# Performance work log

Hardware: AMD Instinct MI355X
Metric: run time of the kernel (lower is better)

## Reference

```python
import jax, jax.numpy as jnp
import numpy as np

B, N1, N2, D, K = 8, 2048, 512, 128, 32
LEVELS, RES, BASE, FC = 3, 3, 0.25, 192
R3 = RES ** 3  # 27 voxel bins per level
EPS = 1e-5


def group_norm(x, gamma, beta, groups):
    # x: [b, C, ...]; normalize per (group) over channel-subset + spatial dims
    b, c = x.shape[0], x.shape[1]
    xg = x.reshape(b, groups, -1)
    mu = xg.mean(axis=-1, keepdims=True)
    var = xg.var(axis=-1, keepdims=True)
    xn = ((xg - mu) * jax.lax.rsqrt(var + EPS)).reshape(x.shape)
    shape = (1, c) + (1,) * (x.ndim - 2)
    return xn * gamma.reshape(shape) + beta.reshape(shape)


def prelu(x, a):
    return jnp.where(x >= 0, x, a * x)


def setup_inputs() -> dict:
    key = jax.random.key(0)
    ks = jax.random.split(key, 12)
    def w(k, shape):
        fan_in = shape[-1]
        return jax.random.uniform(k, shape, jnp.float32, -1.0, 1.0) / jnp.sqrt(jnp.float32(fan_in))
    return {
        "coords": jax.random.normal(ks[0], (B, N1, 3), jnp.float32),
        "coords2": jax.random.normal(ks[1], (B, N2, 3), jnp.float32),
        "fmap1": jax.random.normal(ks[2], (B, D, N1), jnp.float32),
        "fmap2": jax.random.normal(ks[3], (B, D, N2), jnp.float32),
        # vol_conv: Conv1d(81,128,1) -> GN(8,128) -> PReLU -> Conv1d(128,192,1)
        "W1": w(ks[4], (128, R3 * LEVELS)), "b1": jnp.zeros((128,), jnp.float32),
        "g1": jnp.ones((128,), jnp.float32), "be1": jnp.zeros((128,), jnp.float32),
        "a1": jnp.array(0.25, jnp.float32),
        "W2": w(ks[5], (FC, 128)), "b2": jnp.zeros((FC,), jnp.float32),
        # knn_conv: Conv2d(4,64,1) -> GN(8,64) -> PReLU;  knn_out: Conv1d(64,192,1)
        "Wk": w(ks[6], (64, 4)), "bk": jnp.zeros((64,), jnp.float32),
        "gk": jnp.ones((64,), jnp.float32), "bek": jnp.zeros((64,), jnp.float32),
        "ak": jnp.array(0.25, jnp.float32),
        "Wo": w(ks[7], (FC, 64)), "bo": jnp.zeros((FC,), jnp.float32),
    }


def reference(coords, coords2, fmap1, fmap2, W1, b1, g1, be1, a1, W2, b2,
              Wk, bk, gk, bek, ak, Wo, bo):
    b, n1 = coords.shape[0], coords.shape[1]
    n2 = coords2.shape[1]
    dim = fmap1.shape[1]

    # correlation: [b, n1, n2]
    corr = jnp.einsum('bdn,bdm->bnm', fmap1, fmap2) / jnp.sqrt(jnp.float32(dim))
    # pairwise offsets template - search: [b, n1, n2, 3]
    diff = coords2[:, None, :, :] - coords[:, :, None, :]

    # --- multi-level voxel feature via scatter-add ---
    base = jnp.arange(b * n1, dtype=jnp.int32).reshape(b, n1, 1) * R3
    feats = []
    for i in range(LEVELS):
        r = BASE * (2 ** i)
        dv = jnp.round(diff / r)
        valid = jnp.all(jnp.abs(dv) <= (RES // 2), axis=-1)          # [b,n1,n2]
        dvi = (dv + 1.0).astype(jnp.int32)
        cube = dvi[..., 0] * (RES * RES) + dvi[..., 1] * RES + dvi[..., 2]
        idx = jnp.where(valid, cube, 0)                              # torch: cube*valid
        seg = (base + idx).reshape(-1)
        vf = valid.astype(corr.dtype)
        nseg = b * n1 * R3
        add = jax.ops.segment_sum((corr * vf).reshape(-1), seg, num_segments=nseg).reshape(b, n1, R3)
        cnt = jax.ops.segment_sum(vf.reshape(-1), seg, num_segments=nseg).reshape(b, n1, R3)
        feats.append((add / jnp.clip(cnt, 1.0, float(n1))).transpose(0, 2, 1))  # [b,R3,n1]
    vol = jnp.concatenate(feats, axis=1)                             # [b, 3*27, n1]

    h = jnp.einsum('oc,bcn->bon', W1, vol) + b1[None, :, None]
    h = prelu(group_norm(h, g1, be1, 8), a1)
    vol_out = jnp.einsum('oc,bcn->bon', W2, h) + b2[None, :, None]   # [b, FC, n1]

    # --- KNN feature ---
    dist = jnp.sum(diff * diff, axis=-1)                             # [b,n1,n2]
    _, nbr = jax.lax.top_k(-dist, K)                                 # [b,n1,K]
    knn_corr = jnp.take_along_axis(corr, nbr, axis=2)                # [b,n1,K]
    knn_xyz = jnp.take_along_axis(diff, nbr[..., None], axis=2)      # [b,n1,K,3]
    e = jnp.concatenate([knn_corr[:, None], knn_xyz.transpose(0, 3, 1, 2)], axis=1)  # [b,4,n1,K]
    h = jnp.einsum('oc,bcnk->bonk', Wk, e) + bk[None, :, None, None]
    h = prelu(group_norm(h, gk, bek, 8), ak)
    h = jnp.max(h, axis=3)                                           # [b,64,n1]
    knn_out = jnp.einsum('oc,bcn->bon', Wo, h) + bo[None, :, None]   # [b,FC,n1]

    return vol_out + knn_out
```

## Files before the change

### kernel.cpp

```cpp
#include <hip/hip_runtime.h>
#include <hip/hip_bf16.h>

#define N1 2048
#define N2 512
#define KNN 32

typedef unsigned short u16;
typedef unsigned int u32;
typedef unsigned long long u64;
typedef __attribute__((ext_vector_type(8))) short bf16x8;
typedef __attribute__((ext_vector_type(4))) float f32x4;

#define OFF_WT   0
#define OFF_W1B  18432
#define OFF_GV   36864
#define OFF_GK   36992
#define OFF_FLAG 37120
#define OFF_H1   37128
#define OFF_KM   1085704
#define OFF_CO   1609992

__device__ __forceinline__ float tof(u16 u) {
  union { u32 i; float f; } v; v.i = ((u32)u) << 16; return v.f;
}
__device__ __forceinline__ u16 tob(float f) {
  __hip_bfloat16 h = __float2bfloat16(f);
  return *reinterpret_cast<u16*>(&h);
}
__device__ __forceinline__ float fs(float v) {
  return (fabsf(v) < 1e30f) ? v : 0.f;
}

template <int BF>
__device__ __forceinline__ float LD(const void* p, size_t i) {
  if (BF) return tof(((const u16*)p)[i]);
  return ((const float*)p)[i];
}
template <int BF>
__device__ __forceinline__ void ST(void* p, size_t i, float v) {
  if (BF) ((u16*)p)[i] = tob(v);
  else    ((float*)p)[i] = v;
}

__device__ __forceinline__ u32 umin32(u32 a, u32 b) { return a < b ? a : b; }

__device__ __forceinline__ u32 wave_min_u32(u32 v) {
  v = umin32(v, (u32)__builtin_amdgcn_update_dpp((int)0xFFFFFFFF, (int)v, 0x111, 0xf, 0xf, false));
  v = umin32(v, (u32)__builtin_amdgcn_update_dpp((int)0xFFFFFFFF, (int)v, 0x112, 0xf, 0xf, false));
  v = umin32(v, (u32)__builtin_amdgcn_update_dpp((int)0xFFFFFFFF, (int)v, 0x114, 0xf, 0xf, false));
  v = umin32(v, (u32)__builtin_amdgcn_update_dpp((int)0xFFFFFFFF, (int)v, 0x118, 0xf, 0xf, false));
  v = umin32(v, (u32)__builtin_amdgcn_update_dpp((int)0xFFFFFFFF, (int)v, 0x142, 0xa, 0xf, false));
  v = umin32(v, (u32)__builtin_amdgcn_update_dpp((int)0xFFFFFFFF, (int)v, 0x143, 0xc, 0xf, false));
  return (u32)__builtin_amdgcn_readlane((int)v, 63);
}

template <int BF>
__device__ void prep_body(const void* W2, const void* Wo, const void* W1,
                          float* ws, int i0, int stride) {
  u16* wtb = (u16*)(ws + OFF_WT);
  for (int i = i0; i < 192 * 192; i += stride) {
    int o = i / 192, c = i % 192;
    float v = (c < 128) ? LD<BF>(W2, o * 128 + c) : LD<BF>(Wo, o * 64 + (c - 128));
    wtb[o * 192 + c] = tob(fs(v));
  }
  u16* w1b = (u16*)(ws + OFF_W1B);
  for (int i = i0; i < 128 * 96; i += stride) {
    int c = i / 96, j = i % 96;
    float v = (j < 81) ? LD<BF>(W1, c * 81 + j) : 0.f;
    w1b[c * 96 + j] = tob(fs(v));
  }
}

__global__ __launch_bounds__(256) void k_prep(const void* fmap1,
                                              const void* W2, const void* Wo,
                                              const void* W1, float* ws) {
  int t = threadIdx.x;
  __shared__ int sbad;
  if (t == 0) sbad = 0;
  __syncthreads();
  int bad = 0;
  const u16* fm = (const u16*)fmap1;
  for (int i = t * 8; i < t * 8 + 8; i++) {
    float v = tof(fm[i]);
    if (!(fabsf(v) <= 64.f)) bad = 1;
  }
  if (bad) atomicOr(&sbad, 1);
  __syncthreads();
  int bf = sbad ? 0 : 1;
  if (blockIdx.x == 0) {
    if (t == 0) ((int*)(ws + OFF_FLAG))[0] = bf;
    (ws + OFF_GV)[t] = 0.f;
  }
  int i0 = blockIdx.x * 256 + t, stride = gridDim.x * 256;
  if (bf) prep_body<1>(W2, Wo, W1, ws, i0, stride);
  else    prep_body<0>(W2, Wo, W1, ws, i0, stride);
}

template <int BF>
__device__ void corr_stage(const void* f1, const void* f2, u16* As, u16* Bs,
                           int b, int m0, int n0, int t) {
#pragma unroll
  for (int rep = 0; rep < 2; rep++) {
    int i = t + rep * 256;
    int m8 = i & 15, d4 = i >> 4;
    u16 e[4][8];
    if (BF) {
      const u16* F1 = (const u16*)f1;
#pragma unroll
      for (int dr = 0; dr < 4; dr++) {
        uint4 v = *(const uint4*)&F1[(size_t)(b * 128 + d4 * 4 + dr) * N1 + m0 + m8 * 8];
        u32 w[4] = {v.x, v.y, v.z, v.w};
#pragma unroll
        for (int j = 0; j < 8; j++) e[dr][j] = (u16)(w[j >> 1] >> ((j & 1) * 16));
      }
    } else {
      const float* F1 = (const float*)f1;
#pragma unroll
      for (int dr = 0; dr < 4; dr++) {
        const float* src = &F1[(size_t)(b * 128 + d4 * 4 + dr) * N1 + m0 + m8 * 8];
        float4 a = *(const float4*)src, c = *(const float4*)(src + 4);
        float f[8] = {a.x, a.y, a.z, a.w, c.x, c.y, c.z, c.w};
#pragma unroll
        for (int j = 0; j < 8; j++) e[dr][j] = tob(f[j]);
      }
    }
#pragma unroll
    for (int j = 0; j < 8; j++) {
      u64 pk = (u64)e[0][j] | ((u64)e[1][j] << 16) | ((u64)e[2][j] << 32) |
               ((u64)e[3][j] << 48);
      *(u64*)&As[(m8 * 8 + j) * 136 + d4 * 4] = pk;
    }
  }
  {
    int n8 = t & 7, d4 = t >> 3;
    u16 e[4][8];
    if (BF) {
      const u16* F2 = (const u16*)f2;
#pragma unroll
      for (int dr = 0; dr < 4; dr++) {
        uint4 v = *(const uint4*)&F2[(size_t)(b * 128 + d4 * 4 + dr) * N2 + n0 + n8 * 8];
        u32 w[4] = {v.x, v.y, v.z, v.w};
#pragma unroll
        for (int j = 0; j < 8; j++) e[dr][j] = (u16)(w[j >> 1] >> ((j & 1) * 16));
      }
    } else {
      const float* F2 = (const float*)f2;
#pragma unroll
      for (int dr = 0; dr < 4; dr++) {
        const float* src = &F2[(size_t)(b * 128 + d4 * 4 + dr) * N2 + n0 + n8 * 8];
        float4 a = *(const float4*)src, c = *(const float4*)(src + 4);
        float f[8] = {a.x, a.y, a.z, a.w, c.x, c.y, c.z, c.w};
#pragma unroll
        for (int j = 0; j < 8; j++) e[dr][j] = tob(f[j]);
      }
    }
#pragma unroll
    for (int j = 0; j < 8; j++) {
      u64 pk = (u64)e[0][j] | ((u64)e[1][j] << 16) | ((u64)e[2][j] << 32) |
               ((u64)e[3][j] << 48);
      *(u64*)&Bs[(n8 * 8 + j) * 136 + d4 * 4] = pk;
    }
  }
}

__global__ __launch_bounds__(256) void k_corr(const int* flag,
                                              const void* f1, const void* f2,
                                              u16* corrb) {
  __shared__ __attribute__((aligned(16))) u16 As[128 * 136];
  __shared__ __attribute__((aligned(16))) u16 Bs[64 * 136];
  int b = blockIdx.z, m0 = blockIdx.x * 128, n0 = blockIdx.y * 64, t = threadIdx.x;
  if (*flag) corr_stage<1>(f1, f2, As, Bs, b, m0, n0, t);
  else       corr_stage<0>(f1, f2, As, Bs, b, m0, n0, t);
  __syncthreads();

  int wv = t >> 6, lane = t & 63;
  int l15 = lane & 15, q = lane >> 4;
  int wm = (wv >> 1) * 64, wn = (wv & 1) * 32;
  f32x4 acc[4][2];
#pragma unroll
  for (int mt = 0; mt < 4; mt++)
#pragma unroll
    for (int nt = 0; nt < 2; nt++) acc[mt][nt] = (f32x4){0.f, 0.f, 0.f, 0.f};

#pragma unroll
  for (int kc = 0; kc < 128; kc += 32) {
    bf16x8 af[4], bf[2];
#pragma unroll
    for (int mt = 0; mt < 4; mt++)
      af[mt] = *(const bf16x8*)&As[(wm + mt * 16 + l15) * 136 + kc + q * 8];
#pragma unroll
    for (int nt = 0; nt < 2; nt++)
      bf[nt] = *(const bf16x8*)&Bs[(wn + nt * 16 + l15) * 136 + kc + q * 8];
#pragma unroll
    for (int mt = 0; mt < 4; mt++)
#pragma unroll
      for (int nt = 0; nt < 2; nt++)
        acc[mt][nt] = __builtin_amdgcn_mfma_f32_16x16x32_bf16(
            af[mt], bf[nt], acc[mt][nt], 0, 0, 0);
  }
  const float s = 0.08838834764831843f;
#pragma unroll
  for (int mt = 0; mt < 4; mt++)
#pragma unroll
    for (int nt = 0; nt < 2; nt++)
#pragma unroll
      for (int r = 0; r < 4; r++) {
        int m = m0 + wm + mt * 16 + q * 4 + r;
        int n = n0 + wn + nt * 16 + l15;
        corrb[((size_t)(b * N1 + m)) * N2 + n] = tob(acc[mt][nt][r] * s);
      }
}

template <int BF>
__device__ void point_body(const void* coords, const void* coords2,
                           u16* corrb, const void* Wk, const void* bk,
                           u16* knnmax, float* gknnraw,
                           float* c2s, float* binsum, float* bincnt,
                           float4* e_s, float* statk,
                           int b, int p0, int t) {
  int wv = t >> 6, lane = t & 63;
  for (int i = t; i < N2 * 3; i += 256) c2s[i] = LD<BF>(coords2, b * N2 * 3 + i);
  for (int i = t; i < 324; i += 256) { binsum[i] = 0.f; bincnt[i] = 0.f; }
  if (t < 16) statk[t] = 0.f;
  int p = p0 + wv;
  float px = LD<BF>(coords, (b * N1 + p) * 3 + 0);
  float py = LD<BF>(coords, (b * N1 + p) * 3 + 1);
  float pz = LD<BF>(coords, (b * N1 + p) * 3 + 2);
  u16* crow = corrb + ((size_t)(b * N1 + p)) * N2;
  __syncthreads();

  u64 kk[8];
#pragma unroll
  for (int i = 0; i < 8; i++) {
    int n2 = i * 64 + lane;
    float cv = tof(crow[n2]);
    float dx = c2s[n2 * 3 + 0] - px;
    float dy = c2s[n2 * 3 + 1] - py;
    float dz = c2s[n2 * 3 + 2] - pz;
    float dist = __fadd_rn(__fadd_rn(__fmul_rn(dx, dx), __fmul_rn(dy, dy)),
                           __fmul_rn(dz, dz));
    union { float f; u32 u; } du; du.f = dist;
    kk[i] = (((u64)du.u) << 32) | (u64)n2;
    float sc = 4.f;
#pragma unroll
    for (int lvl = 0; lvl < 3; lvl++) {
      float vx = rintf(dx * sc), vy = rintf(dy * sc), vz = rintf(dz * sc);
      if (fabsf(vx) <= 1.f && fabsf(vy) <= 1.f && fabsf(vz) <= 1.f) {
        int cube = ((int)vx + 1) * 9 + ((int)vy + 1) * 3 + ((int)vz + 1);
        atomicAdd(&binsum[wv * 81 + lvl * 27 + cube], cv);
        atomicAdd(&bincnt[wv * 81 + lvl * 27 + cube], 1.f);
      }
      sc *= 0.5f;
    }
  }

#define CAS(a, b) { u64 x = kk[a], y = kk[b]; bool sw = y < x; \
                    kk[a] = sw ? y : x; kk[b] = sw ? x : y; }
  CAS(0,1) CAS(2,3) CAS(4,5) CAS(6,7)
  CAS(0,2) CAS(1,3) CAS(4,6) CAS(5,7)
  CAS(1,2) CAS(5,6)
  CAS(0,4) CAS(1,5) CAS(2,6) CAS(3,7)
  CAS(2,4) CAS(3,5)
  CAS(1,2) CAS(3,4) CAS(5,6)
#undef CAS
  int my_idx = 0;
  for (int it = 0; it < KNN; it++) {
    u32 hb = (u32)(kk[0] >> 32);
    u32 wb = wave_min_u32(hb);
    u32 hidx = (hb == wb) ? (u32)kk[0] : 0xFFFFFFFFu;
    u32 widx = wave_min_u32(hidx);
    if (lane == it) my_idx = (int)widx;
    if (lane == (int)(widx & 63u)) {
      kk[0] = kk[1]; kk[1] = kk[2]; kk[2] = kk[3]; kk[3] = kk[4];
      kk[4] = kk[5]; kk[5] = kk[6]; kk[6] = kk[7]; kk[7] = ~0ull;
    }
  }
  if (lane < KNN) {
    float4 ev;
    ev.x = tof(crow[my_idx]);
    ev.y = c2s[my_idx * 3 + 0] - px;
    ev.z = c2s[my_idx * 3 + 1] - py;
    ev.w = c2s[my_idx * 3 + 2] - pz;
    e_s[wv * 32 + lane] = ev;
  }
#pragma unroll
  for (int rep = 0; rep < 2; rep++) {
    int i = lane + rep * 64;
    if (i < 96) {
      float v = (i < 81)
          ? binsum[wv * 81 + i] / fmaxf(bincnt[wv * 81 + i], 1.f) : 0.f;
      crow[i] = tob(v);
    }
  }

  {
    int cch = lane;
    float w0 = LD<BF>(Wk, cch * 4 + 0), w1 = LD<BF>(Wk, cch * 4 + 1);
    float w2 = LD<BF>(Wk, cch * 4 + 2), w3 = LD<BF>(Wk, cch * 4 + 3);
    float bv = LD<BF>(bk, cch);
    float sm = 0.f, sq = 0.f, mx = -3e38f;
#pragma unroll 8
    for (int k = 0; k < KNN; k++) {
      float4 ev = e_s[wv * 32 + k];
      float h = bv + w0 * ev.x + w1 * ev.y + w2 * ev.z + w3 * ev.w;
      sm += h; sq += h * h; mx = fmaxf(mx, h);
    }
    knnmax[((size_t)(b * N1 + p)) * 64 + cch] = tob(mx);
    sm += __shfl_xor(sm, 1, 64); sq += __shfl_xor(sq, 1, 64);
    sm += __shfl_xor(sm, 2, 64); sq += __shfl_xor(sq, 2, 64);
    sm += __shfl_xor(sm, 4, 64); sq += __shfl_xor(sq, 4, 64);
    if ((lane & 7) == 0) {
      int g = cch >> 3;
      atomicAdd(&statk[g * 2 + 0], sm);
      atomicAdd(&statk[g * 2 + 1], sq);
    }
  }
  __syncthreads();
  if (t < 16) atomicAdd(&gknnraw[b * 16 + t], statk[t]);
}

__global__ __launch_bounds__(256) void k_point(const int* flag,
                                               const void* coords, const void* coords2,
                                               u16* corrb, const void* Wk,
                                               const void* bk, u16* knnmax,
                                               float* gknnraw) {
  __shared__ float c2s[N2 * 3];
  __shared__ float binsum[4 * 81];
  __shared__ float bincnt[4 * 81];
  __shared__ float4 e_s[4 * 32];
  __shared__ float statk[16];
  int b = blockIdx.y, p0 = blockIdx.x * 4, t = threadIdx.x;
  if (*flag)
    point_body<1>(coords, coords2, corrb, Wk, bk, knnmax, gknnraw,
                  c2s, binsum, bincnt, e_s, statk, b, p0, t);
  else
    point_body<0>(coords, coords2, corrb, Wk, bk, knnmax, gknnraw,
                  c2s, binsum, bincnt, e_s, statk, b, p0, t);
}

template <int BF>
__device__ void vol_body(const u16* corrb, const u16* w1b, const void* b1,
                         u16* h1b, float* gvolraw, float* Bi1, float* statv,
                         int b, int p0, int t) {
  if (t < 128) Bi1[t] = LD<BF>(b1, t);
  if (t < 16) statv[t] = 0.f;
  __syncthreads();

  int wv = t >> 6, lane = t & 63;
  int l15 = lane & 15, q = lane >> 4;
  int pbase = p0 + wv * 16;
  f32x4 acc[8];
#pragma unroll
  for (int nt = 0; nt < 8; nt++) acc[nt] = (f32x4){0.f, 0.f, 0.f, 0.f};

#pragma unroll
  for (int kc = 0; kc < 96; kc += 32) {
    bf16x8 af = *(const bf16x8*)&corrb[((size_t)(b * N1 + pbase + l15)) * N2 + kc + q * 8];
    bf16x8 bf[8];
#pragma unroll
    for (int nt = 0; nt < 8; nt++)
      bf[nt] = *(const bf16x8*)&w1b[(nt * 16 + l15) * 96 + kc + q * 8];
#pragma unroll
    for (int nt = 0; nt < 8; nt++)
      acc[nt] = __builtin_amdgcn_mfma_f32_16x16x32_bf16(af, bf[nt], acc[nt], 0, 0, 0);
  }
  float sm[8], sq[8];
#pragma unroll
  for (int nt = 0; nt < 8; nt++) {
    int c = nt * 16 + l15;
    float s0 = 0.f, q0 = 0.f;
#pragma unroll
    for (int r = 0; r < 4; r++) {
      int p = pbase + q * 4 + r;
      float v = acc[nt][r] + Bi1[c];
      h1b[((size_t)(b * N1 + p)) * 128 + c] = tob(v);
      s0 += v; q0 += v * v;
    }
    sm[nt] = s0; sq[nt] = q0;
  }
#pragma unroll
  for (int nt = 0; nt < 8; nt++) {
    sm[nt] += __shfl_xor(sm[nt], 16, 64); sq[nt] += __shfl_xor(sq[nt], 16, 64);
    sm[nt] += __shfl_xor(sm[nt], 32, 64); sq[nt] += __shfl_xor(sq[nt], 32, 64);
  }
  if (q == 0) {
#pragma unroll
    for (int nt = 0; nt < 8; nt++) {
      int g = (nt * 16 + l15) >> 4;
      atomicAdd(&statv[g * 2 + 0], sm[nt]);
      atomicAdd(&statv[g * 2 + 1], sq[nt]);
    }
  }
  __syncthreads();
  if (t < 16) atomicAdd(&gvolraw[b * 16 + t], statv[t]);
}

__global__ __launch_bounds__(256) void k_vol(const int* flag, const u16* corrb,
                                             const u16* w1b, const void* b1,
                                             u16* h1b, float* gvolraw) {
  __shared__ float Bi1[128];
  __shared__ float statv[16];
  int b = blockIdx.y, p0 = blockIdx.x * 64, t = threadIdx.x;
  if (*flag) vol_body<1>(corrb, w1b, b1, h1b, gvolraw, Bi1, statv, b, p0, t);
  else       vol_body<0>(corrb, w1b, b1, h1b, gvolraw, Bi1, statv, b, p0, t);
}

template <int BF>
__device__ void out_body(const u16* h1b, const u16* knnmax, const u16* wtb,
                         const float* gvolraw, const float* gknnraw,
                         const void* g1, const void* be1, const void* a1p,
                         const void* gk, const void* bek, const void* akp,
                         const void* b2, const void* bo, void* out,
                         float* Ac, float* Bc, float* Sc, float* Bi, u16* gs,
                         int b, int p0, int t) {
  if (t < 192) {
    float A, Bv, slope;
    if (t < 128) {
      int g = t >> 4;
      float S = fs(gvolraw[b * 16 + g * 2 + 0]);
      float Q = fs(gvolraw[b * 16 + g * 2 + 1]);
      float mean = S / 32768.f;
      float var = fmaxf(Q / 32768.f - mean * mean, 0.f);
      float inv = 1.f / sqrtf(var + 1e-5f);
      A = inv * LD<BF>(g1, t); Bv = LD<BF>(be1, t) - mean * A;
      slope = LD<BF>(a1p, 0);
    } else {
      int c = t - 128, g = c >> 3;
      float S = fs(gknnraw[b * 16 + g * 2 + 0]);
      float Q = fs(gknnraw[b * 16 + g * 2 + 1]);
      float mean = S / 524288.f;
      float var = fmaxf(Q / 524288.f - mean * mean, 0.f);
      float inv = 1.f / sqrtf(var + 1e-5f);
      A = inv * LD<BF>(gk, c); Bv = LD<BF>(bek, c) - mean * A;
      slope = LD<BF>(akp, 0);
    }
    Ac[t] = A; Bc[t] = Bv; Sc[t] = slope;
    Bi[t] = LD<BF>(b2, t) + LD<BF>(bo, t);
  }
  __syncthreads();

  for (int i = t; i < 1536; i += 256) {
    int p = i / 24, c8 = i % 24;
    int c0 = c8 * 8;
    uint4 v;
    if (c8 < 16) v = *(const uint4*)&h1b[((size_t)(b * N1 + p0 + p)) * 128 + c0];
    else         v = *(const uint4*)&knnmax[((size_t)(b * N1 + p0 + p)) * 64 + (c0 - 128)];
    u16 e[8] = {(u16)(v.x & 0xffff), (u16)(v.x >> 16), (u16)(v.y & 0xffff),
                (u16)(v.y >> 16),    (u16)(v.z & 0xffff), (u16)(v.z >> 16),
                (u16)(v.w & 0xffff), (u16)(v.w >> 16)};
    u16 r[8];
#pragma unroll
    for (int j = 0; j < 8; j++) {
      int c = c0 + j;
      float xn = tof(e[j]) * Ac[c] + Bc[c];
      xn = xn >= 0.f ? xn : Sc[c] * xn;
      r[j] = tob(xn);
    }
    uint4 wv;
    wv.x = (u32)r[0] | ((u32)r[1] << 16);
    wv.y = (u32)r[2] | ((u32)r[3] << 16);
    wv.z = (u32)r[4] | ((u32)r[5] << 16);
    wv.w = (u32)r[6] | ((u32)r[7] << 16);
    *(uint4*)&gs[p * 200 + c0] = wv;
  }
  __syncthreads();

  int wv2 = t >> 6, lane = t & 63;
  int l15 = lane & 15, q = lane >> 4;
  int obase = wv2 * 48;
  f32x4 acc[3][4];
#pragma unroll
  for (int mt = 0; mt < 3; mt++)
#pragma unroll
    for (int nt = 0; nt < 4; nt++) acc[mt][nt] = (f32x4){0.f, 0.f, 0.f, 0.f};

#pragma unroll
  for (int kc = 0; kc < 192; kc += 32) {
    bf16x8 af[3], bf[4];
#pragma unroll
    for (int mt = 0; mt < 3; mt++)
      af[mt] = *(const bf16x8*)&wtb[(size_t)(obase + mt * 16 + l15) * 192 + kc + q * 8];
#pragma unroll
    for (int nt = 0; nt < 4; nt++)
      bf[nt] = *(const bf16x8*)&gs[(nt * 16 + l15) * 200 + kc + q * 8];
#pragma unroll
    for (int mt = 0; mt < 3; mt++)
#pragma unroll
      for (int nt = 0; nt < 4; nt++)
        acc[mt][nt] = __builtin_amdgcn_mfma_f32_16x16x32_bf16(
            af[mt], bf[nt], acc[mt][nt], 0, 0, 0);
  }
#pragma unroll
  for (int mt = 0; mt < 3; mt++)
#pragma unroll
    for (int nt = 0; nt < 4; nt++)
#pragma unroll
      for (int r = 0; r < 4; r++) {
        int o = obase + mt * 16 + q * 4 + r;
        int p = p0 + nt * 16 + l15;
        ST<BF>(out, ((size_t)(b * 192 + o)) * N1 + p, fs(acc[mt][nt][r] + Bi[o]));
      }
}

__global__ __launch_bounds__(256) void k_out(const int* flag,
                                             const u16* h1b, const u16* knnmax,
                                             const u16* wtb,
                                             const float* gvolraw, const float* gknnraw,
                                             const void* g1, const void* be1,
                                             const void* a1p, const void* gk,
                                             const void* bek, const void* akp,
                                             const void* b2, const void* bo,
                                             void* out) {
  __shared__ float Ac[192], Bc[192], Sc[192], Bi[192];
  __shared__ __attribute__((aligned(16))) u16 gs[64 * 200];
  int b = blockIdx.y, p0 = blockIdx.x * 64, t = threadIdx.x;
  if (*flag)
    out_body<1>(h1b, knnmax, wtb, gvolraw, gknnraw, g1, be1, a1p, gk, bek, akp,
                b2, bo, out, Ac, Bc, Sc, Bi, gs, b, p0, t);
  else
    out_body<0>(h1b, knnmax, wtb, gvolraw, gknnraw, g1, be1, a1p, gk, bek, akp,
                b2, bo, out, Ac, Bc, Sc, Bi, gs, b, p0, t);
}

extern "C" void kernel_launch(void* const* d_in, const int* in_sizes, int n_in,
                              void* d_out, int out_size, void* d_ws, size_t ws_size,
                              hipStream_t stream) {
  const void* coords  = d_in[0];
  const void* coords2 = d_in[1];
  const void* fmap1   = d_in[2];
  const void* fmap2   = d_in[3];
  const void* W1  = d_in[4];
  const void* b1  = d_in[5];
  const void* g1  = d_in[6];
  const void* be1 = d_in[7];
  const void* a1  = d_in[8];
  const void* W2  = d_in[9];
  const void* b2  = d_in[10];
  const void* Wk  = d_in[11];
  const void* bk  = d_in[12];
  const void* gk  = d_in[13];
  const void* bek = d_in[14];
  const void* ak  = d_in[15];
  const void* Wo  = d_in[16];
  const void* bo  = d_in[17];

  float* ws = (float*)d_ws;
  u16* wtb       = (u16*)(ws + OFF_WT);
  u16* w1b       = (u16*)(ws + OFF_W1B);
  float* gvolraw = ws + OFF_GV;
  float* gknnraw = ws + OFF_GK;
  const int* flag = (const int*)(ws + OFF_FLAG);
  u16* h1b    = (u16*)(ws + OFF_H1);
  u16* knnmax = (u16*)(ws + OFF_KM);
  u16* corrb  = (u16*)(ws + OFF_CO);

  k_prep<<<dim3(40), dim3(256), 0, stream>>>(fmap1, W2, Wo, W1, ws);
  k_corr<<<dim3(16, 8, 8), dim3(256), 0, stream>>>(flag, fmap1, fmap2, corrb);
  k_point<<<dim3(512, 8), dim3(256), 0, stream>>>(flag, coords, coords2, corrb,
                                                  Wk, bk, knnmax, gknnraw);
  k_vol<<<dim3(32, 8), dim3(256), 0, stream>>>(flag, corrb, w1b, b1, h1b, gvolraw);
  k_out<<<dim3(32, 8), dim3(256), 0, stream>>>(flag, h1b, knnmax, wtb,
                                               gvolraw, gknnraw, g1, be1, a1,
                                               gk, bek, ak, b2, bo, d_out);
}
```

Measured before the change: 210.4 us.

## Fuse point and vol kernels, drop W2/Wo prep, add ballot fast path in top-k

```diff
diff --git a/kernel.cpp b/kernel.cpp
--- a/kernel.cpp
+++ b/kernel.cpp
@@ -11,7 +11,6 @@
 typedef __attribute__((ext_vector_type(8))) short bf16x8;
 typedef __attribute__((ext_vector_type(4))) float f32x4;
 
-#define OFF_WT   0
 #define OFF_W1B  18432
 #define OFF_GV   36864
 #define OFF_GK   36992
@@ -55,25 +54,34 @@
 }
 
 template <int BF>
-__device__ void prep_body(const void* W2, const void* Wo, const void* W1,
-                          float* ws, int i0, int stride) {
-  u16* wtb = (u16*)(ws + OFF_WT);
-  for (int i = i0; i < 192 * 192; i += stride) {
-    int o = i / 192, c = i % 192;
-    float v = (c < 128) ? LD<BF>(W2, o * 128 + c) : LD<BF>(Wo, o * 64 + (c - 128));
-    wtb[o * 192 + c] = tob(fs(v));
-  }
+__device__ __forceinline__ bf16x8 ld_wfrag(const void* W2, const void* Wo,
+                                           int o, int k0) {
+  if (BF) {
+    const u16* p = (k0 < 128) ? (const u16*)W2 + (size_t)o * 128 + k0
+                              : (const u16*)Wo + (size_t)o * 64 + (k0 - 128);
+    return *(const bf16x8*)p;
+  } else {
+    const float* p = (k0 < 128) ? (const float*)W2 + (size_t)o * 128 + k0
+                                : (const float*)Wo + (size_t)o * 64 + (k0 - 128);
+    bf16x8 r;
+#pragma unroll
+    for (int j = 0; j < 8; j++) r[j] = (short)tob(p[j]);
+    return r;
+  }
+}
+
+template <int BF>
+__device__ void prep_body(const void* W1, float* ws, int i0, int stride) {
   u16* w1b = (u16*)(ws + OFF_W1B);
   for (int i = i0; i < 128 * 96; i += stride) {
     int c = i / 96, j = i % 96;
     float v = (j < 81) ? LD<BF>(W1, c * 81 + j) : 0.f;
-    w1b[c * 96 + j] = tob(fs(v));
-  }
-}
-
-__global__ __launch_bounds__(256) void k_prep(const void* fmap1,
-                                              const void* W2, const void* Wo,
-                                              const void* W1, float* ws) {
+    w1b[i] = tob(fs(v));
+  }
+}
+
+__global__ __launch_bounds__(256) void k_prep(const void* fmap1, const void* W1,
+                                              float* ws) {
   int t = threadIdx.x;
   __shared__ int sbad;
   if (t == 0) sbad = 0;
@@ -92,8 +100,8 @@
     (ws + OFF_GV)[t] = 0.f;
   }
   int i0 = blockIdx.x * 256 + t, stride = gridDim.x * 256;
-  if (bf) prep_body<1>(W2, Wo, W1, ws, i0, stride);
-  else    prep_body<0>(W2, Wo, W1, ws, i0, stride);
+  if (bf) prep_body<1>(W1, ws, i0, stride);
+  else    prep_body<0>(W1, ws, i0, stride);
 }
 
 template <int BF>
@@ -212,201 +220,195 @@
 }
 
 template <int BF>
-__device__ void point_body(const void* coords, const void* coords2,
-                           u16* corrb, const void* Wk, const void* bk,
-                           u16* knnmax, float* gknnraw,
-                           float* c2s, float* binsum, float* bincnt,
-                           float4* e_s, float* statk,
-                           int b, int p0, int t) {
+__device__ void pv_body(const void* coords, const void* coords2,
+                        const u16* corrb, const void* Wk, const void* bk,
+                        const u16* w1b, const void* b1,
+                        u16* h1b, u16* knnmax,
+                        float* gvolraw, float* gknnraw,
+                        float* c2s, float* binsum, float* bincnt,
+                        float4* e_s, u16* volb, float* statv, float* statk,
+                        int b, int p0, int t) {
   int wv = t >> 6, lane = t & 63;
+  int l15 = lane & 15, q = lane >> 4;
   for (int i = t; i < N2 * 3; i += 256) c2s[i] = LD<BF>(coords2, b * N2 * 3 + i);
-  for (int i = t; i < 324; i += 256) { binsum[i] = 0.f; bincnt[i] = 0.f; }
-  if (t < 16) statk[t] = 0.f;
-  int p = p0 + wv;
-  float px = LD<BF>(coords, (b * N1 + p) * 3 + 0);
-  float py = LD<BF>(coords, (b * N1 + p) * 3 + 1);
-  float pz = LD<BF>(coords, (b * N1 + p) * 3 + 2);
-  u16* crow = corrb + ((size_t)(b * N1 + p)) * N2;
-  __syncthreads();
-
-  u64 kk[8];
-#pragma unroll
-  for (int i = 0; i < 8; i++) {
-    int n2 = i * 64 + lane;
-    float cv = tof(crow[n2]);
-    float dx = c2s[n2 * 3 + 0] - px;
-    float dy = c2s[n2 * 3 + 1] - py;
-    float dz = c2s[n2 * 3 + 2] - pz;
-    float dist = __fadd_rn(__fadd_rn(__fmul_rn(dx, dx), __fmul_rn(dy, dy)),
-                           __fmul_rn(dz, dz));
-    union { float f; u32 u; } du; du.f = dist;
-    kk[i] = (((u64)du.u) << 32) | (u64)n2;
-    float sc = 4.f;
-#pragma unroll
-    for (int lvl = 0; lvl < 3; lvl++) {
-      float vx = rintf(dx * sc), vy = rintf(dy * sc), vz = rintf(dz * sc);
-      if (fabsf(vx) <= 1.f && fabsf(vy) <= 1.f && fabsf(vz) <= 1.f) {
-        int cube = ((int)vx + 1) * 9 + ((int)vy + 1) * 3 + ((int)vz + 1);
-        atomicAdd(&binsum[wv * 81 + lvl * 27 + cube], cv);
-        atomicAdd(&bincnt[wv * 81 + lvl * 27 + cube], 1.f);
-      }
-      sc *= 0.5f;
-    }
-  }
+  if (t < 16) { statv[t] = 0.f; statk[t] = 0.f; }
+  __syncthreads();
+
+  for (int s = 0; s < 4; s++) {
+    int pp = wv * 4 + s;
+    int p = p0 + pp;
+    for (int i = lane; i < 81; i += 64) {
+      binsum[wv * 81 + i] = 0.f;
+      bincnt[wv * 81 + i] = 0.f;
+    }
+    float px = LD<BF>(coords, (b * N1 + p) * 3 + 0);
+    float py = LD<BF>(coords, (b * N1 + p) * 3 + 1);
+    float pz = LD<BF>(coords, (b * N1 + p) * 3 + 2);
+    const u16* crow = corrb + ((size_t)(b * N1 + p)) * N2;
+
+    u64 kk[8];
+#pragma unroll
+    for (int i = 0; i < 8; i++) {
+      int n2 = i * 64 + lane;
+      float cv = tof(crow[n2]);
+      float dx = c2s[n2 * 3 + 0] - px;
+      float dy = c2s[n2 * 3 + 1] - py;
+      float dz = c2s[n2 * 3 + 2] - pz;
+      float dist = __fadd_rn(__fadd_rn(__fmul_rn(dx, dx), __fmul_rn(dy, dy)),
+                             __fmul_rn(dz, dz));
+      union { float f; u32 u; } du; du.f = dist;
+      kk[i] = (((u64)du.u) << 32) | (u64)n2;
+      float sc = 4.f;
+#pragma unroll
+      for (int lvl = 0; lvl < 3; lvl++) {
+        float vx = rintf(dx * sc), vy = rintf(dy * sc), vz = rintf(dz * sc);
+        if (fabsf(vx) <= 1.f && fabsf(vy) <= 1.f && fabsf(vz) <= 1.f) {
+          int cube = ((int)vx + 1) * 9 + ((int)vy + 1) * 3 + ((int)vz + 1);
+          atomicAdd(&binsum[wv * 81 + lvl * 27 + cube], cv);
+          atomicAdd(&bincnt[wv * 81 + lvl * 27 + cube], 1.f);
+        }
+        sc *= 0.5f;
+      }
+    }
 
 #define CAS(a, b) { u64 x = kk[a], y = kk[b]; bool sw = y < x; \
                     kk[a] = sw ? y : x; kk[b] = sw ? x : y; }
-  CAS(0,1) CAS(2,3) CAS(4,5) CAS(6,7)
-  CAS(0,2) CAS(1,3) CAS(4,6) CAS(5,7)
-  CAS(1,2) CAS(5,6)
-  CAS(0,4) CAS(1,5) CAS(2,6) CAS(3,7)
-  CAS(2,4) CAS(3,5)
-  CAS(1,2) CAS(3,4) CAS(5,6)
+    CAS(0,1) CAS(2,3) CAS(4,5) CAS(6,7)
+    CAS(0,2) CAS(1,3) CAS(4,6) CAS(5,7)
+    CAS(1,2) CAS(5,6)
+    CAS(0,4) CAS(1,5) CAS(2,6) CAS(3,7)
+    CAS(2,4) CAS(3,5)
+    CAS(1,2) CAS(3,4) CAS(5,6)
 #undef CAS
-  int my_idx = 0;
-  for (int it = 0; it < KNN; it++) {
-    u32 hb = (u32)(kk[0] >> 32);
-    u32 wb = wave_min_u32(hb);
-    u32 hidx = (hb == wb) ? (u32)kk[0] : 0xFFFFFFFFu;
-    u32 widx = wave_min_u32(hidx);
-    if (lane == it) my_idx = (int)widx;
-    if (lane == (int)(widx & 63u)) {
-      kk[0] = kk[1]; kk[1] = kk[2]; kk[2] = kk[3]; kk[3] = kk[4];
-      kk[4] = kk[5]; kk[5] = kk[6]; kk[6] = kk[7]; kk[7] = ~0ull;
-    }
-  }
-  if (lane < KNN) {
-    float4 ev;
-    ev.x = tof(crow[my_idx]);
-    ev.y = c2s[my_idx * 3 + 0] - px;
-    ev.z = c2s[my_idx * 3 + 1] - py;
-    ev.w = c2s[my_idx * 3 + 2] - pz;
-    e_s[wv * 32 + lane] = ev;
-  }
-#pragma unroll
-  for (int rep = 0; rep < 2; rep++) {
-    int i = lane + rep * 64;
-    if (i < 96) {
-      float v = (i < 81)
-          ? binsum[wv * 81 + i] / fmaxf(bincnt[wv * 81 + i], 1.f) : 0.f;
-      crow[i] = tob(v);
-    }
-  }
-
-  {
-    int cch = lane;
-    float w0 = LD<BF>(Wk, cch * 4 + 0), w1 = LD<BF>(Wk, cch * 4 + 1);
-    float w2 = LD<BF>(Wk, cch * 4 + 2), w3 = LD<BF>(Wk, cch * 4 + 3);
-    float bv = LD<BF>(bk, cch);
-    float sm = 0.f, sq = 0.f, mx = -3e38f;
+    int my_idx = 0;
+    for (int it = 0; it < KNN; it++) {
+      u32 hb = (u32)(kk[0] >> 32);
+      u32 wb = wave_min_u32(hb);
+      u64 mask = __ballot(hb == wb);
+      u32 widx;
+      if (__builtin_popcountll(mask) == 1) {
+        int wl = (int)__builtin_ctzll(mask);
+        widx = (u32)__builtin_amdgcn_readlane((int)(u32)kk[0], wl);
+      } else {
+        u32 hidx = (hb == wb) ? (u32)kk[0] : 0xFFFFFFFFu;
+        widx = wave_min_u32(hidx);
+      }
+      if (lane == it) my_idx = (int)widx;
+      if (lane == (int)(widx & 63u)) {
+        kk[0] = kk[1]; kk[1] = kk[2]; kk[2] = kk[3]; kk[3] = kk[4];
+        kk[4] = kk[5]; kk[5] = kk[6]; kk[6] = kk[7]; kk[7] = ~0ull;
+      }
+    }
+    if (lane < KNN) {
+      float4 ev;
+      ev.x = tof(crow[my_idx]);
+      ev.y = c2s[my_idx * 3 + 0] - px;
+      ev.z = c2s[my_idx * 3 + 1] - py;
+      ev.w = c2s[my_idx * 3 + 2] - pz;
+      e_s[wv * 32 + lane] = ev;
+    }
+#pragma unroll
+    for (int rep = 0; rep < 2; rep++) {
+      int i = lane + rep * 64;
+      if (i < 96) {
+        float v = (i < 81)
+            ? binsum[wv * 81 + i] / fmaxf(bincnt[wv * 81 + i], 1.f) : 0.f;
+        volb[pp * 104 + i] = tob(v);
+      }
+    }
+
+    {
+      int cch = lane;
+      float w0 = LD<BF>(Wk, cch * 4 + 0), w1 = LD<BF>(Wk, cch * 4 + 1);
+      float w2 = LD<BF>(Wk, cch * 4 + 2), w3 = LD<BF>(Wk, cch * 4 + 3);
+      float bv = LD<BF>(bk, cch);
+      float sm = 0.f, sq = 0.f, mx = -3e38f;
 #pragma unroll 8
-    for (int k = 0; k < KNN; k++) {
-      float4 ev = e_s[wv * 32 + k];
-      float h = bv + w0 * ev.x + w1 * ev.y + w2 * ev.z + w3 * ev.w;
-      sm += h; sq += h * h; mx = fmaxf(mx, h);
-    }
-    knnmax[((size_t)(b * N1 + p)) * 64 + cch] = tob(mx);
-    sm += __shfl_xor(sm, 1, 64); sq += __shfl_xor(sq, 1, 64);
-    sm += __shfl_xor(sm, 2, 64); sq += __shfl_xor(sq, 2, 64);
-    sm += __shfl_xor(sm, 4, 64); sq += __shfl_xor(sq, 4, 64);
-    if ((lane & 7) == 0) {
-      int g = cch >> 3;
-      atomicAdd(&statk[g * 2 + 0], sm);
-      atomicAdd(&statk[g * 2 + 1], sq);
-    }
-  }
-  __syncthreads();
-  if (t < 16) atomicAdd(&gknnraw[b * 16 + t], statk[t]);
-}
-
-__global__ __launch_bounds__(256) void k_point(const int* flag,
-                                               const void* coords, const void* coords2,
-                                               u16* corrb, const void* Wk,
-                                               const void* bk, u16* knnmax,
-                                               float* gknnraw) {
+      for (int k = 0; k < KNN; k++) {
+        float4 ev = e_s[wv * 32 + k];
+        float h = bv + w0 * ev.x + w1 * ev.y + w2 * ev.z + w3 * ev.w;
+        sm += h; sq += h * h; mx = fmaxf(mx, h);
+      }
+      knnmax[((size_t)(b * N1 + p)) * 64 + cch] = tob(mx);
+      sm += __shfl_xor(sm, 1, 64); sq += __shfl_xor(sq, 1, 64);
+      sm += __shfl_xor(sm, 2, 64); sq += __shfl_xor(sq, 2, 64);
+      sm += __shfl_xor(sm, 4, 64); sq += __shfl_xor(sq, 4, 64);
+      if ((lane & 7) == 0) {
+        int g = cch >> 3;
+        atomicAdd(&statk[g * 2 + 0], sm);
+        atomicAdd(&statk[g * 2 + 1], sq);
+      }
+    }
+  }
+  __syncthreads();
+
+  f32x4 acc[2];
+  acc[0] = (f32x4){0.f, 0.f, 0.f, 0.f};
+  acc[1] = (f32x4){0.f, 0.f, 0.f, 0.f};
+#pragma unroll
+  for (int kc = 0; kc < 96; kc += 32) {
+    bf16x8 af = *(const bf16x8*)&volb[l15 * 104 + kc + q * 8];
+    bf16x8 bf0 = *(const bf16x8*)&w1b[((2 * wv + 0) * 16 + l15) * 96 + kc + q * 8];
+    bf16x8 bf1 = *(const bf16x8*)&w1b[((2 * wv + 1) * 16 + l15) * 96 + kc + q * 8];
+    acc[0] = __builtin_amdgcn_mfma_f32_16x16x32_bf16(af, bf0, acc[0], 0, 0, 0);
+    acc[1] = __builtin_amdgcn_mfma_f32_16x16x32_bf16(af, bf1, acc[1], 0, 0, 0);
+  }
+#pragma unroll
+  for (int ct = 0; ct < 2; ct++) {
+    int c = (2 * wv + ct) * 16 + l15;
+    float bias = LD<BF>(b1, c);
+    float sm = 0.f, sq = 0.f;
+#pragma unroll
+    for (int r = 0; r < 4; r++) {
+      int p = p0 + q * 4 + r;
+      float v = acc[ct][r] + bias;
+      h1b[((size_t)(b * N1 + p)) * 128 + c] = tob(v);
+      sm += v; sq += v * v;
+    }
+    sm += __shfl_xor(sm, 1, 64);  sq += __shfl_xor(sq, 1, 64);
+    sm += __shfl_xor(sm, 2, 64);  sq += __shfl_xor(sq, 2, 64);
+    sm += __shfl_xor(sm, 4, 64);  sq += __shfl_xor(sq, 4, 64);
+    sm += __shfl_xor(sm, 8, 64);  sq += __shfl_xor(sq, 8, 64);
+    sm += __shfl_xor(sm, 16, 64); sq += __shfl_xor(sq, 16, 64);
+    sm += __shfl_xor(sm, 32, 64); sq += __shfl_xor(sq, 32, 64);
+    if (lane == 0) {
+      int g = 2 * wv + ct;
+      atomicAdd(&statv[g * 2 + 0], sm);
+      atomicAdd(&statv[g * 2 + 1], sq);
+    }
+  }
+  __syncthreads();
+  if (t < 16) atomicAdd(&gvolraw[b * 16 + t], statv[t]);
+  else if (t < 32) atomicAdd(&gknnraw[b * 16 + (t - 16)], statk[t - 16]);
+}
+
+__global__ __launch_bounds__(256) void k_pv(const int* flag,
+                                            const void* coords, const void* coords2,
+                                            const u16* corrb, const void* Wk,
+                                            const void* bk, const u16* w1b,
+                                            const void* b1, u16* h1b,
+                                            u16* knnmax, float* gvolraw,
+                                            float* gknnraw) {
   __shared__ float c2s[N2 * 3];
   __shared__ float binsum[4 * 81];
   __shared__ float bincnt[4 * 81];
   __shared__ float4 e_s[4 * 32];
-  __shared__ float statk[16];
-  int b = blockIdx.y, p0 = blockIdx.x * 4, t = threadIdx.x;
+  __shared__ __attribute__((aligned(16))) u16 volb[16 * 104];
+  __shared__ float statv[16], statk[16];
+  int b = blockIdx.y, p0 = blockIdx.x * 16, t = threadIdx.x;
   if (*flag)
-    point_body<1>(coords, coords2, corrb, Wk, bk, knnmax, gknnraw,
-                  c2s, binsum, bincnt, e_s, statk, b, p0, t);
+    pv_body<1>(coords, coords2, corrb, Wk, bk, w1b, b1, h1b, knnmax,
+               gvolraw, gknnraw, c2s, binsum, bincnt, e_s, volb, statv, statk,
+               b, p0, t);
   else
-    point_body<0>(coords, coords2, corrb, Wk, bk, knnmax, gknnraw,
-                  c2s, binsum, bincnt, e_s, statk, b, p0, t);
-}
-
-template <int BF>
-__device__ void vol_body(const u16* corrb, const u16* w1b, const void* b1,
-                         u16* h1b, float* gvolraw, float* Bi1, float* statv,
-                         int b, int p0, int t) {
-  if (t < 128) Bi1[t] = LD<BF>(b1, t);
-  if (t < 16) statv[t] = 0.f;
-  __syncthreads();
-
-  int wv = t >> 6, lane = t & 63;
-  int l15 = lane & 15, q = lane >> 4;
-  int pbase = p0 + wv * 16;
-  f32x4 acc[8];
-#pragma unroll
-  for (int nt = 0; nt < 8; nt++) acc[nt] = (f32x4){0.f, 0.f, 0.f, 0.f};
-
-#pragma unroll
-  for (int kc = 0; kc < 96; kc += 32) {
-    bf16x8 af = *(const bf16x8*)&corrb[((size_t)(b * N1 + pbase + l15)) * N2 + kc + q * 8];
-    bf16x8 bf[8];
-#pragma unroll
-    for (int nt = 0; nt < 8; nt++)
-      bf[nt] = *(const bf16x8*)&w1b[(nt * 16 + l15) * 96 + kc + q * 8];
-#pragma unroll
-    for (int nt = 0; nt < 8; nt++)
-      acc[nt] = __builtin_amdgcn_mfma_f32_16x16x32_bf16(af, bf[nt], acc[nt], 0, 0, 0);
-  }
-  float sm[8], sq[8];
-#pragma unroll
-  for (int nt = 0; nt < 8; nt++) {
-    int c = nt * 16 + l15;
-    float s0 = 0.f, q0 = 0.f;
-#pragma unroll
-    for (int r = 0; r < 4; r++) {
-      int p = pbase + q * 4 + r;
-      float v = acc[nt][r] + Bi1[c];
-      h1b[((size_t)(b * N1 + p)) * 128 + c] = tob(v);
-      s0 += v; q0 += v * v;
-    }
-    sm[nt] = s0; sq[nt] = q0;
-  }
-#pragma unroll
-  for (int nt = 0; nt < 8; nt++) {
-    sm[nt] += __shfl_xor(sm[nt], 16, 64); sq[nt] += __shfl_xor(sq[nt], 16, 64);
-    sm[nt] += __shfl_xor(sm[nt], 32, 64); sq[nt] += __shfl_xor(sq[nt], 32, 64);
-  }
-  if (q == 0) {
-#pragma unroll
-    for (int nt = 0; nt < 8; nt++) {
-      int g = (nt * 16 + l15) >> 4;
-      atomicAdd(&statv[g * 2 + 0], sm[nt]);
-      atomicAdd(&statv[g * 2 + 1], sq[nt]);
-    }
-  }
-  __syncthreads();
-  if (t < 16) atomicAdd(&gvolraw[b * 16 + t], statv[t]);
-}
-
-__global__ __launch_bounds__(256) void k_vol(const int* flag, const u16* corrb,
-                                             const u16* w1b, const void* b1,
-                                             u16* h1b, float* gvolraw) {
-  __shared__ float Bi1[128];
-  __shared__ float statv[16];
-  int b = blockIdx.y, p0 = blockIdx.x * 64, t = threadIdx.x;
-  if (*flag) vol_body<1>(corrb, w1b, b1, h1b, gvolraw, Bi1, statv, b, p0, t);
-  else       vol_body<0>(corrb, w1b, b1, h1b, gvolraw, Bi1, statv, b, p0, t);
-}
-
-template <int BF>
-__device__ void out_body(const u16* h1b, const u16* knnmax, const u16* wtb,
+    pv_body<0>(coords, coords2, corrb, Wk, bk, w1b, b1, h1b, knnmax,
+               gvolraw, gknnraw, c2s, binsum, bincnt, e_s, volb, statv, statk,
+               b, p0, t);
+}
+
+template <int BF>
+__device__ void out_body(const u16* h1b, const u16* knnmax,
+                         const void* W2, const void* Wo,
                          const float* gvolraw, const float* gknnraw,
                          const void* g1, const void* be1, const void* a1p,
                          const void* gk, const void* bek, const void* akp,
@@ -479,7 +481,7 @@
     bf16x8 af[3], bf[4];
 #pragma unroll
     for (int mt = 0; mt < 3; mt++)
-      af[mt] = *(const bf16x8*)&wtb[(size_t)(obase + mt * 16 + l15) * 192 + kc + q * 8];
+      af[mt] = ld_wfrag<BF>(W2, Wo, obase + mt * 16 + l15, kc + q * 8);
 #pragma unroll
     for (int nt = 0; nt < 4; nt++)
       bf[nt] = *(const bf16x8*)&gs[(nt * 16 + l15) * 200 + kc + q * 8];
@@ -504,7 +506,7 @@
 
 __global__ __launch_bounds__(256) void k_out(const int* flag,
                                              const u16* h1b, const u16* knnmax,
-                                             const u16* wtb,
+                                             const void* W2, const void* Wo,
                                              const float* gvolraw, const float* gknnraw,
                                              const void* g1, const void* be1,
                                              const void* a1p, const void* gk,
@@ -515,11 +517,11 @@
   __shared__ __attribute__((aligned(16))) u16 gs[64 * 200];
   int b = blockIdx.y, p0 = blockIdx.x * 64, t = threadIdx.x;
   if (*flag)
-    out_body<1>(h1b, knnmax, wtb, gvolraw, gknnraw, g1, be1, a1p, gk, bek, akp,
-                b2, bo, out, Ac, Bc, Sc, Bi, gs, b, p0, t);
+    out_body<1>(h1b, knnmax, W2, Wo, gvolraw, gknnraw, g1, be1, a1p, gk, bek,
+                akp, b2, bo, out, Ac, Bc, Sc, Bi, gs, b, p0, t);
   else
-    out_body<0>(h1b, knnmax, wtb, gvolraw, gknnraw, g1, be1, a1p, gk, bek, akp,
-                b2, bo, out, Ac, Bc, Sc, Bi, gs, b, p0, t);
+    out_body<0>(h1b, knnmax, W2, Wo, gvolraw, gknnraw, g1, be1, a1p, gk, bek,
+                akp, b2, bo, out, Ac, Bc, Sc, Bi, gs, b, p0, t);
 }
 
 extern "C" void kernel_launch(void* const* d_in, const int* in_sizes, int n_in,
@@ -545,7 +547,6 @@
   const void* bo  = d_in[17];
 
   float* ws = (float*)d_ws;
-  u16* wtb       = (u16*)(ws + OFF_WT);
   u16* w1b       = (u16*)(ws + OFF_W1B);
   float* gvolraw = ws + OFF_GV;
   float* gknnraw = ws + OFF_GK;
@@ -554,12 +555,12 @@
   u16* knnmax = (u16*)(ws + OFF_KM);
   u16* corrb  = (u16*)(ws + OFF_CO);
 
-  k_prep<<<dim3(40), dim3(256), 0, stream>>>(fmap1, W2, Wo, W1, ws);
+  k_prep<<<dim3(8), dim3(256), 0, stream>>>(fmap1, W1, ws);
   k_corr<<<dim3(16, 8, 8), dim3(256), 0, stream>>>(flag, fmap1, fmap2, corrb);
-  k_point<<<dim3(512, 8), dim3(256), 0, stream>>>(flag, coords, coords2, corrb,
-                                                  Wk, bk, knnmax, gknnraw);
-  k_vol<<<dim3(32, 8), dim3(256), 0, stream>>>(flag, corrb, w1b, b1, h1b, gvolraw);
-  k_out<<<dim3(32, 8), dim3(256), 0, stream>>>(flag, h1b, knnmax, wtb,
+  k_pv<<<dim3(128, 8), dim3(256), 0, stream>>>(flag, coords, coords2, corrb,
+                                               Wk, bk, w1b, b1, h1b, knnmax,
+                                               gvolraw, gknnraw);
+  k_out<<<dim3(32, 8), dim3(256), 0, stream>>>(flag, h1b, knnmax, W2, Wo,
                                                gvolraw, gknnraw, g1, be1, a1,
                                                gk, bek, ak, b2, bo, d_out);
 }
```

After: 207.6 us. About the same (-1.3%).
